# Optimization experiments

Measured on AMD Instinct MI355X. Metric: run time of the kernel, lower is better.

## Reference

```python
import jax, jax.numpy as jnp
import numpy as np

N = 6000          # num nodes (max_nodes)
E = 192000        # num edges
NTYPES = 100
NCLUST = 4        # hardcoded num_nodes=4 in diff_pool_net.__init__
OUT = 16
BN_EPS = 1e-5

PARAM_SHAPES = {
    'emb_w': (NTYPES, 64),
    # gnn1_pool: GNN(64, 64, 4, lin=True); DenseSAGEConv: lin_rel (no bias) + lin_root (bias)
    'pw1r': (64, 64), 'pw1l': (64, 64), 'pb1': (64,),
    'pw2r': (64, 64), 'pw2l': (64, 64), 'pb2': (64,),
    'pw3r': (NCLUST, 64), 'pw3l': (NCLUST, 64), 'pb3': (NCLUST,),
    'plin_w': (NCLUST, 2 * 64 + NCLUST), 'plin_b': (NCLUST,),
    # gnn1_embed: GNN(64, 64, 64, lin=False)
    'ew1r': (64, 64), 'ew1l': (64, 64), 'eb1': (64,),
    'ew2r': (64, 64), 'ew2l': (64, 64), 'eb2': (64,),
    'ew3r': (64, 64), 'ew3l': (64, 64), 'eb3': (64,),
    'lin1_w': (64, 192), 'lin1_b': (64,),
    'lin2_w': (OUT, 64), 'lin2_b': (OUT,),
    'embl_w': (32, 192), 'embl_b': (32,),
    'lin3_w': (OUT, 32 + OUT), 'lin3_b': (OUT,),
}


def _lin(x, w, b=None):
    y = x @ w.T
    return y if b is None else y + b


def _sage(x, adj, wr, wl, b):
    # DenseSAGEConv: mean-aggregate over dense adj, then lin_rel(agg) + lin_root(x)
    agg = jnp.matmul(adj, x)
    deg = jnp.clip(jnp.sum(adj, axis=-1, keepdims=True), 1.0, None)
    return _lin(agg / deg, wr) + _lin(x, wl, b)


def _bn(x):
    # training-mode BatchNorm1d with default gamma=1, beta=0 (biased variance)
    c = x.shape[-1]
    xf = x.reshape(-1, c)
    m = jnp.mean(xf, axis=0)
    v = jnp.var(xf, axis=0)
    return ((xf - m) * jax.lax.rsqrt(v + BN_EPS)).reshape(x.shape)


def _gnn(x, adj, wr1, wl1, b1, wr2, wl2, b2, wr3, wl3, b3, lw=None, lb=None):
    x1 = _bn(jax.nn.relu(_sage(x, adj, wr1, wl1, b1)))
    x2 = _bn(jax.nn.relu(_sage(x1, adj, wr2, wl2, b2)))
    x3 = _bn(jax.nn.relu(_sage(x2, adj, wr3, wl3, b3)))
    xc = jnp.concatenate([x1, x2, x3], axis=-1)
    if lw is not None:
        xc = jax.nn.relu(_lin(xc, lw, lb))
    return xc


def _forward(p, edge_index, node_types):
    # to_dense_adj: scatter-add edges into a dense [1, N, N] adjacency
    adj = jnp.zeros((N, N), jnp.float32).at[edge_index[0], edge_index[1]].add(1.0)[None]
    x = p['emb_w'][node_types][None]                      # [1, N, 64]
    s = _gnn(x, adj, p['pw1r'], p['pw1l'], p['pb1'],
             p['pw2r'], p['pw2l'], p['pb2'],
             p['pw3r'], p['pw3l'], p['pb3'],
             p['plin_w'], p['plin_b'])                    # [1, N, 4]
    xe = _gnn(x, adj, p['ew1r'], p['ew1l'], p['eb1'],
              p['ew2r'], p['ew2l'], p['eb2'],
              p['ew3r'], p['ew3l'], p['eb3'])             # [1, N, 192]
    x_embed = _lin(xe, p['embl_w'], p['embl_b'])          # [1, N, 32]
    # dense_diff_pool pooled features: softmax(S)^T @ X (pooled adj/losses are unused downstream)
    ssm = jax.nn.softmax(s, axis=-1)
    s_x = jnp.einsum('bnk,bnc->bkc', ssm, xe)             # [1, 4, 192]
    s_x = jax.nn.relu(_lin(s_x, p['lin1_w'], p['lin1_b']))
    s_x = _lin(s_x, p['lin2_w'], p['lin2_b'])             # [1, 4, OUT]
    # one_hot=True branch: per-node gather of its cluster row (vectorized form of the python loop)
    idx = jnp.argmax(s, axis=-1)                          # [1, N]
    res = jnp.take(s_x[0], idx[0], axis=0)[None]          # [1, N, OUT]
    return _lin(jnp.concatenate([x_embed, res], axis=-1), p['lin3_w'], p['lin3_b'])


def setup_inputs() -> dict:
    key = jax.random.key(0)
    ks = jax.random.split(key, len(PARAM_SHAPES) + 2)
    inp = {n: jax.random.normal(k, shp, jnp.float32) * 0.1
           for (n, shp), k in zip(PARAM_SHAPES.items(), ks)}
    inp['edge_index'] = jax.random.randint(ks[-2], (2, E), 0, N)
    inp['node_types'] = jax.random.randint(ks[-1], (N,), 0, NTYPES)
    return inp


def reference(edge_index, node_types, emb_w, pw1r, pw1l, pb1, pw2r, pw2l, pb2,
              pw3r, pw3l, pb3, plin_w, plin_b, ew1r, ew1l, eb1, ew2r, ew2l, eb2,
              ew3r, ew3l, eb3, lin1_w, lin1_b, lin2_w, lin2_b, embl_w, embl_b,
              lin3_w, lin3_b):
    args = locals()
    p = {k: args[k] for k in PARAM_SHAPES}
    return _forward(p, edge_index, node_types)
```

## Files before the change

### kernel.cpp

```cpp
#include <hip/hip_runtime.h>
#include <hip/hip_bf16.h>

#define NN 6000
#define EE 192000

#define W_DEG     0
#define W_CUR     6000
#define W_STATS   12000
#define W_SXACC   12768
#define W_ZEND    13536
#define W_FLAG    13536
#define W_ROWPTR  13540
#define W_COL     19544
#define W_X0      211544
#define W_ZP1     595544
#define W_ZP2     979544
#define W_ZP3     1363544
#define W_ZE1     1387544
#define W_ZE2     1771544
#define W_ZE3     2155544
#define W_S       2539544
#define W_SX2     2563544
#define W_PAR     2563608

struct PtrTab {
  const void* src[29];
  int off[29];
  int cnt[29];
};

__device__ __forceinline__ float bf2f(unsigned short h) {
  return __uint_as_float(((unsigned)h) << 16);
}
__device__ __forceinline__ int rfl(int x) { return __builtin_amdgcn_readfirstlane(x); }

__global__ void k_detect(const void* emb, int* flag) {
  __shared__ int bad;
  if (threadIdx.x == 0) bad = 0;
  __syncthreads();
  const unsigned short* p = (const unsigned short*)emb;
  float v0 = bf2f(p[threadIdx.x]);
  float v1 = bf2f(p[threadIdx.x + 256]);
  if (!(fabsf(v0) <= 100.f) || !(fabsf(v1) <= 100.f)) bad = 1;
  __syncthreads();
  if (threadIdx.x == 0) flag[0] = bad ? 0 : 1;
}

__global__ void k_convert(PtrTab tab, float* base, const int* flag) {
  int b = blockIdx.x;
  const void* s = tab.src[b];
  float* d = base + tab.off[b];
  int n = tab.cnt[b];
  bool bf = (flag[0] == 1);
  if (bf) {
    const unsigned short* sp = (const unsigned short*)s;
    for (int i = threadIdx.x; i < n; i += 256) d[i] = bf2f(sp[i]);
  } else {
    const float* sp = (const float*)s;
    for (int i = threadIdx.x; i < n; i += 256) d[i] = sp[i];
  }
}

__global__ void k_deg(const int* __restrict__ ei, int* __restrict__ deg) {
  int e = blockIdx.x * 256 + threadIdx.x;
  if (e < EE) atomicAdd(&deg[ei[e]], 1);
}

__global__ void k_scan(const int* __restrict__ deg, int* __restrict__ rowptr) {
  __shared__ int part[1024];
  int t = threadIdx.x;
  int base = t * 6;
  int loc[6]; int s = 0;
#pragma unroll
  for (int j = 0; j < 6; ++j) { int i = base + j; int v = (i < NN) ? deg[i] : 0; loc[j] = s; s += v; }
  part[t] = s;
  __syncthreads();
  for (int off = 1; off < 1024; off <<= 1) {
    int v = part[t];
    int add = (t >= off) ? part[t - off] : 0;
    __syncthreads();
    part[t] = v + add;
    __syncthreads();
  }
  int pre = (t == 0) ? 0 : part[t - 1];
#pragma unroll
  for (int j = 0; j < 6; ++j) { int i = base + j; if (i <= NN) rowptr[i] = pre + loc[j]; }
}

__global__ void k_scatter(const int* __restrict__ ei, const int* __restrict__ rowptr,
                          int* __restrict__ cur, int* __restrict__ col) {
  int e = blockIdx.x * 256 + threadIdx.x;
  if (e < EE) {
    int s = ei[e], d = ei[EE + e];
    int pos = atomicAdd(&cur[s], 1);
    col[rowptr[s] + pos] = d;
  }
}

__global__ void k_emb(const float* __restrict__ emb, const int* __restrict__ nt, float* __restrict__ x0) {
  int t = blockIdx.x * 256 + threadIdx.x;
  int i = t >> 4, q = t & 15;
  *(float4*)&x0[i * 64 + q * 4] = *(const float4*)&emb[nt[i] * 64 + q * 4];
}

template <int OUT, bool HS>
__device__ __forceinline__ void sage_body(
    const float* __restrict__ in_z, const float* __restrict__ in_stats,
    const float* __restrict__ wr, const float* __restrict__ wl, const float* __restrict__ bias,
    const int* __restrict__ rowptr, const int* __restrict__ col,
    float* __restrict__ out_z, float* __restrict__ out_stats,
    int vb, int total_waves,
    float* __restrict__ wrT, float* __restrict__ wlT, float* __restrict__ bs,
    float (* __restrict__ vec)[2][64], float (* __restrict__ red)[2][64]) {
  int tid = threadIdx.x, lane = tid & 63, wv = tid >> 6;

  for (int i = tid; i < 64 * OUT; i += 256) {
    int f = i >> 6, k = i & 63;
    wrT[k * (OUT + 1) + f] = wr[i];
    wlT[k * (OUT + 1) + f] = wl[i];
  }
  if (tid < OUT) bs[tid] = bias[tid];

  int quad = lane & 15, sub = lane >> 4;
  float m = 0.f, r = 1.f;
  float m4x = 0.f, m4y = 0.f, m4z = 0.f, m4w = 0.f;
  float r4x = 1.f, r4y = 1.f, r4z = 1.f, r4w = 1.f;
  if (HS) {
    float s = in_stats[lane], q = in_stats[64 + lane];
    m = s * (1.f / NN);
    r = rsqrtf(q * (1.f / NN) - m * m + 1e-5f);
    float4 s4 = *(const float4*)(in_stats + quad * 4);
    float4 q4 = *(const float4*)(in_stats + 64 + quad * 4);
    m4x = s4.x * (1.f / NN); m4y = s4.y * (1.f / NN); m4z = s4.z * (1.f / NN); m4w = s4.w * (1.f / NN);
    r4x = rsqrtf(q4.x * (1.f / NN) - m4x * m4x + 1e-5f);
    r4y = rsqrtf(q4.y * (1.f / NN) - m4y * m4y + 1e-5f);
    r4z = rsqrtf(q4.z * (1.f / NN) - m4z * m4z + 1e-5f);
    r4w = rsqrtf(q4.w * (1.f / NN) - m4w * m4w + 1e-5f);
  }
  __syncthreads();

  float accs = 0.f, accq = 0.f;
  int ol = lane & (OUT - 1);
  int wave_id = vb * 4 + wv;
  for (int n = wave_id; n < NN; n += total_waves) {
    float x = (in_z[n * 64 + lane] - m) * r;
    int rs = rfl(rowptr[n]), re = rfl(rowptr[n + 1]);
    int cnt = re - rs;
    float szx = 0.f, szy = 0.f, szz = 0.f, szw = 0.f;
    for (int base = rs; base < re; base += 32) {
#pragma unroll
      for (int u = 0; u < 8; ++u) {
        int cidx = base + u * 4 + sub;
        bool ok = cidx < re;
        int cc = ok ? cidx : rs;
        int j = col[cc];
        const float4 v = *(const float4*)(in_z + j * 64 + quad * 4);
        if (ok) { szx += v.x; szy += v.y; szz += v.z; szw += v.w; }
      }
    }
#pragma unroll
    for (int off = 16; off < 64; off <<= 1) {
      szx += __shfl_xor(szx, off);
      szy += __shfl_xor(szy, off);
      szz += __shfl_xor(szz, off);
      szw += __shfl_xor(szw, off);
    }
    float inv = 1.f / (float)(cnt > 0 ? cnt : 1);
    float fc = (float)cnt;
    if (sub == 0) {
      float4 a;
      a.x = (szx - fc * m4x) * r4x * inv;
      a.y = (szy - fc * m4y) * r4y * inv;
      a.z = (szz - fc * m4z) * r4z * inv;
      a.w = (szw - fc * m4w) * r4w * inv;
      *(float4*)&vec[wv][0][quad * 4] = a;
    }
    vec[wv][1][lane] = x;
    float y = bs[ol];
    const float* va = &vec[wv][0][0];
    const float* vx = &vec[wv][1][0];
#pragma unroll
    for (int kk = 0; kk < 16; ++kk) {
      const float4 a4 = *(const float4*)(va + kk * 4);
      const float4 x4 = *(const float4*)(vx + kk * 4);
      int k0 = kk * 4;
      y += a4.x * wrT[(k0 + 0) * (OUT + 1) + ol] + x4.x * wlT[(k0 + 0) * (OUT + 1) + ol];
      y += a4.y * wrT[(k0 + 1) * (OUT + 1) + ol] + x4.y * wlT[(k0 + 1) * (OUT + 1) + ol];
      y += a4.z * wrT[(k0 + 2) * (OUT + 1) + ol] + x4.z * wlT[(k0 + 2) * (OUT + 1) + ol];
      y += a4.w * wrT[(k0 + 3) * (OUT + 1) + ol] + x4.w * wlT[(k0 + 3) * (OUT + 1) + ol];
    }
    float z = fmaxf(y, 0.f);
    if (lane < OUT) {
      out_z[n * OUT + lane] = z;
      accs += z; accq += z * z;
    }
  }
  if (lane < OUT) { red[wv][0][lane] = accs; red[wv][1][lane] = accq; }
  __syncthreads();
  if (tid < OUT) {
    float s = red[0][0][tid] + red[1][0][tid] + red[2][0][tid] + red[3][0][tid];
    float q = red[0][1][tid] + red[1][1][tid] + red[2][1][tid] + red[3][1][tid];
    atomicAdd(&out_stats[tid], s);
    atomicAdd(&out_stats[64 + tid], q);
  }
}

template <int OUTA, int OUTB, bool HS>
__global__ __launch_bounds__(256, 4) void k_dual(
    const float* __restrict__ inA, const float* __restrict__ stA,
    const float* __restrict__ wrA, const float* __restrict__ wlA, const float* __restrict__ bA,
    float* __restrict__ outA, float* __restrict__ ostA,
    const float* __restrict__ inB, const float* __restrict__ stB,
    const float* __restrict__ wrB, const float* __restrict__ wlB, const float* __restrict__ bB,
    float* __restrict__ outB, float* __restrict__ ostB,
    const int* __restrict__ rowptr, const int* __restrict__ col, int G) {
  __shared__ float wrT[64 * 65];
  __shared__ float wlT[64 * 65];
  __shared__ float bs[64];
  __shared__ float vec[4][2][64];
  __shared__ float red[4][2][64];
  if ((int)blockIdx.x < G)
    sage_body<OUTA, HS>(inA, stA, wrA, wlA, bA, rowptr, col, outA, ostA,
                        blockIdx.x, G * 4, wrT, wlT, bs, vec, red);
  else
    sage_body<OUTB, HS>(inB, stB, wrB, wlB, bB, rowptr, col, outB, ostB,
                        blockIdx.x - G, G * 4, wrT, wlT, bs, vec, red);
}

__global__ __launch_bounds__(256) void k_pool(
    const float* __restrict__ zp1, const float* __restrict__ zp2, const float* __restrict__ zp3,
    const float* __restrict__ sp1, const float* __restrict__ sp2, const float* __restrict__ sp3,
    const float* __restrict__ ze1, const float* __restrict__ ze2, const float* __restrict__ ze3,
    const float* __restrict__ se1, const float* __restrict__ se2, const float* __restrict__ se3,
    const float* __restrict__ plw, const float* __restrict__ plb,
    float* __restrict__ s_out, float* __restrict__ sx_acc) {
  __shared__ float red[4][12][64];
  int tid = threadIdx.x, lane = tid & 63, wv = tid >> 6;

  float mp1 = sp1[lane] * (1.f / NN); float rp1 = rsqrtf(sp1[64 + lane] * (1.f / NN) - mp1 * mp1 + 1e-5f);
  float mp2 = sp2[lane] * (1.f / NN); float rp2 = rsqrtf(sp2[64 + lane] * (1.f / NN) - mp2 * mp2 + 1e-5f);
  float mp3 = 0.f, rp3 = 1.f;
  if (lane < 4) { mp3 = sp3[lane] * (1.f / NN); rp3 = rsqrtf(sp3[64 + lane] * (1.f / NN) - mp3 * mp3 + 1e-5f); }
  float me1 = se1[lane] * (1.f / NN); float re1 = rsqrtf(se1[64 + lane] * (1.f / NN) - me1 * me1 + 1e-5f);
  float me2 = se2[lane] * (1.f / NN); float re2 = rsqrtf(se2[64 + lane] * (1.f / NN) - me2 * me2 + 1e-5f);
  float me3 = se3[lane] * (1.f / NN); float re3 = rsqrtf(se3[64 + lane] * (1.f / NN) - me3 * me3 + 1e-5f);

  float w0a = plw[0 * 132 + lane], w0b = plw[0 * 132 + 64 + lane], w0c = (lane < 4) ? plw[0 * 132 + 128 + lane] : 0.f;
  float w1a = plw[1 * 132 + lane], w1b = plw[1 * 132 + 64 + lane], w1c = (lane < 4) ? plw[1 * 132 + 128 + lane] : 0.f;
  float w2a = plw[2 * 132 + lane], w2b = plw[2 * 132 + 64 + lane], w2c = (lane < 4) ? plw[2 * 132 + 128 + lane] : 0.f;
  float w3a = plw[3 * 132 + lane], w3b = plw[3 * 132 + 64 + lane], w3c = (lane < 4) ? plw[3 * 132 + 128 + lane] : 0.f;
  float pb0 = plb[0], pb1v = plb[1], pb2v = plb[2], pb3v = plb[3];

  float acc[12];
#pragma unroll
  for (int u = 0; u < 12; ++u) acc[u] = 0.f;

  int wave_id = blockIdx.x * 4 + wv;
  for (int n = wave_id; n < NN; n += 1500) {
    float a = (zp1[n * 64 + lane] - mp1) * rp1;
    float b = (zp2[n * 64 + lane] - mp2) * rp2;
    float c = (lane < 4) ? ((zp3[n * 4 + lane] - mp3) * rp3) : 0.f;
    float p0 = a * w0a + b * w0b + c * w0c;
    float p1 = a * w1a + b * w1b + c * w1c;
    float p2 = a * w2a + b * w2b + c * w2c;
    float p3 = a * w3a + b * w3b + c * w3c;
#pragma unroll
    for (int off = 1; off < 64; off <<= 1) {
      p0 += __shfl_xor(p0, off);
      p1 += __shfl_xor(p1, off);
      p2 += __shfl_xor(p2, off);
      p3 += __shfl_xor(p3, off);
    }
    float s0 = fmaxf(p0 + pb0, 0.f), s1 = fmaxf(p1 + pb1v, 0.f);
    float s2 = fmaxf(p2 + pb2v, 0.f), s3 = fmaxf(p3 + pb3v, 0.f);
    if (lane < 4) {
      float sv = (lane == 0) ? s0 : (lane == 1) ? s1 : (lane == 2) ? s2 : s3;
      s_out[n * 4 + lane] = sv;
    }
    float mx = fmaxf(fmaxf(s0, s1), fmaxf(s2, s3));
    float e0 = __expf(s0 - mx), e1 = __expf(s1 - mx), e2 = __expf(s2 - mx), e3 = __expf(s3 - mx);
    float inv = 1.f / (e0 + e1 + e2 + e3);
    e0 *= inv; e1 *= inv; e2 *= inv; e3 *= inv;
    float x1 = (ze1[n * 64 + lane] - me1) * re1;
    float x2 = (ze2[n * 64 + lane] - me2) * re2;
    float x3 = (ze3[n * 64 + lane] - me3) * re3;
    acc[0] += e0 * x1; acc[1] += e0 * x2; acc[2] += e0 * x3;
    acc[3] += e1 * x1; acc[4] += e1 * x2; acc[5] += e1 * x3;
    acc[6] += e2 * x1; acc[7] += e2 * x2; acc[8] += e2 * x3;
    acc[9] += e3 * x1; acc[10] += e3 * x2; acc[11] += e3 * x3;
  }
#pragma unroll
  for (int u = 0; u < 12; ++u) red[wv][u][lane] = acc[u];
  __syncthreads();
  for (int u = tid; u < 768; u += 256) {
    int f = u & 63, q = u >> 6;
    float v = red[0][q][f] + red[1][q][f] + red[2][q][f] + red[3][q][f];
    int k = q / 3, slot = q - 3 * k;
    atomicAdd(&sx_acc[k * 192 + slot * 64 + f], v);
  }
}

__global__ void k_mlp(const float* __restrict__ sx, const float* __restrict__ l1w, const float* __restrict__ l1b,
                      const float* __restrict__ l2w, const float* __restrict__ l2b, float* __restrict__ sx2) {
  __shared__ float tl[4][64];
  int tid = threadIdx.x;
  int k = tid >> 6, f = tid & 63;
  float v = l1b[f];
  for (int c = 0; c < 192; ++c) v += sx[k * 192 + c] * l1w[f * 192 + c];
  tl[k][f] = fmaxf(v, 0.f);
  __syncthreads();
  if (tid < 64) {
    int kk = tid >> 4, o = tid & 15;
    float u = l2b[o];
#pragma unroll
    for (int j = 0; j < 64; ++j) u += tl[kk][j] * l2w[o * 64 + j];
    sx2[kk * 16 + o] = u;
  }
}

__global__ __launch_bounds__(256) void k_final(
    const float* __restrict__ ze1, const float* __restrict__ ze2, const float* __restrict__ ze3,
    const float* __restrict__ se1, const float* __restrict__ se2, const float* __restrict__ se3,
    const float* __restrict__ ew, const float* __restrict__ ebv,
    const float* __restrict__ l3w, const float* __restrict__ l3b,
    const float* __restrict__ s_out, const float* __restrict__ sx2,
    const int* __restrict__ flag, void* __restrict__ out) {
  __shared__ float ewT[192 * 33];
  __shared__ float l3T[48 * 17];
  __shared__ float ebs[32], l3bs[16];
  __shared__ float xev[4][192];
  __shared__ float xed[4][32];
  int tid = threadIdx.x, lane = tid & 63, wv = tid >> 6;

  for (int i = tid; i < 6144; i += 256) { int cp = i / 192, c = i - cp * 192; ewT[c * 33 + cp] = ew[i]; }
  for (int i = tid; i < 768; i += 256) { int o = i / 48, j = i - o * 48; l3T[j * 17 + o] = l3w[i]; }
  if (tid < 32) ebs[tid] = ebv[tid];
  if (tid < 16) l3bs[tid] = l3b[tid];

  float me1 = se1[lane] * (1.f / NN); float re1 = rsqrtf(se1[64 + lane] * (1.f / NN) - me1 * me1 + 1e-5f);
  float me2 = se2[lane] * (1.f / NN); float re2 = rsqrtf(se2[64 + lane] * (1.f / NN) - me2 * me2 + 1e-5f);
  float me3 = se3[lane] * (1.f / NN); float re3 = rsqrtf(se3[64 + lane] * (1.f / NN) - me3 * me3 + 1e-5f);
  bool bf = (flag[0] == 1);
  __syncthreads();

  int h = lane >> 5, L = lane & 31;
  int wave_id = blockIdx.x * 4 + wv;
  for (int n = wave_id; n < NN; n += 2048) {
    float x1 = (ze1[n * 64 + lane] - me1) * re1;
    float x2 = (ze2[n * 64 + lane] - me2) * re2;
    float x3 = (ze3[n * 64 + lane] - me3) * re3;
    xev[wv][lane] = x1;
    xev[wv][64 + lane] = x2;
    xev[wv][128 + lane] = x3;
    float v = (h == 0) ? ebs[L] : 0.f;
    int cb = h * 96;
#pragma unroll
    for (int c4 = 0; c4 < 24; ++c4) {
      const float4 xv = *(const float4*)&xev[wv][cb + c4 * 4];
      int c0 = cb + c4 * 4;
      v += xv.x * ewT[(c0 + 0) * 33 + L];
      v += xv.y * ewT[(c0 + 1) * 33 + L];
      v += xv.z * ewT[(c0 + 2) * 33 + L];
      v += xv.w * ewT[(c0 + 3) * 33 + L];
    }
    v += __shfl_xor(v, 32);
    if (h == 0) xed[wv][L] = v;
    if (lane < 16) {
      int idx = 0; float best = s_out[n * 4 + 0];
      float c1 = s_out[n * 4 + 1]; if (c1 > best) { best = c1; idx = 1; }
      float c2 = s_out[n * 4 + 2]; if (c2 > best) { best = c2; idx = 2; }
      float c3 = s_out[n * 4 + 3]; if (c3 > best) { best = c3; idx = 3; }
      float racc = l3bs[lane];
#pragma unroll
      for (int j = 0; j < 32; ++j) racc += xed[wv][j] * l3T[j * 17 + lane];
      const float* sxr = sx2 + idx * 16;
#pragma unroll
      for (int j = 0; j < 16; ++j) racc += sxr[j] * l3T[(32 + j) * 17 + lane];
      if (bf) ((__hip_bfloat16*)out)[n * 16 + lane] = __float2bfloat16(racc);
      else    ((float*)out)[n * 16 + lane] = racc;
    }
  }
}

extern "C" void kernel_launch(void* const* d_in, const int* in_sizes, int n_in,
                              void* d_out, int out_size, void* d_ws, size_t ws_size,
                              hipStream_t stream) {
  float* F = (float*)d_ws;
  int* I = (int*)d_ws;

  static const int pcnt[29] = {6400, 4096, 4096, 64, 4096, 4096, 64, 256, 256, 4, 528, 4,
                               4096, 4096, 64, 4096, 4096, 64, 4096, 4096, 64,
                               12288, 64, 1024, 16, 6144, 32, 768, 16};
  int poff[29];
  { int a = 0; for (int i = 0; i < 29; ++i) { poff[i] = a; a += pcnt[i]; } }

  PtrTab tab;
  for (int i = 0; i < 29; ++i) { tab.src[i] = d_in[i]; tab.off[i] = poff[i]; tab.cnt[i] = pcnt[i]; }

  const int* ei = (const int*)d_in[29];
  const int* nt = (const int*)d_in[30];

  int* deg = I + W_DEG;
  int* cur = I + W_CUR;
  int* rowptr = I + W_ROWPTR;
  int* col = I + W_COL;
  int* flag = I + W_FLAG;
  float* st = F + W_STATS;
  float* sxacc = F + W_SXACC;
  float* x0 = F + W_X0;
  float* zp1 = F + W_ZP1; float* zp2 = F + W_ZP2; float* zp3 = F + W_ZP3;
  float* ze1 = F + W_ZE1; float* ze2 = F + W_ZE2; float* ze3 = F + W_ZE3;
  float* sbuf = F + W_S;
  float* sx2 = F + W_SX2;
  float* P = F + W_PAR;
#define PP(i) (P + poff[i])

  hipMemsetAsync(d_ws, 0, (size_t)W_ZEND * 4, stream);
  k_detect<<<1, 256, 0, stream>>>(d_in[0], flag);
  k_convert<<<29, 256, 0, stream>>>(tab, P, flag);
  k_deg<<<750, 256, 0, stream>>>(ei, deg);
  k_scan<<<1, 1024, 0, stream>>>(deg, rowptr);
  k_scatter<<<750, 256, 0, stream>>>(ei, rowptr, cur, col);
  k_emb<<<375, 256, 0, stream>>>(PP(0), nt, x0);

  k_dual<64, 64, false><<<1024, 256, 0, stream>>>(
      x0, nullptr, PP(1), PP(2), PP(3), zp1, st + 0 * 128,
      x0, nullptr, PP(12), PP(13), PP(14), ze1, st + 3 * 128,
      rowptr, col, 512);
  k_dual<64, 64, true><<<1024, 256, 0, stream>>>(
      zp1, st + 0 * 128, PP(4), PP(5), PP(6), zp2, st + 1 * 128,
      ze1, st + 3 * 128, PP(15), PP(16), PP(17), ze2, st + 4 * 128,
      rowptr, col, 512);
  k_dual<4, 64, true><<<1024, 256, 0, stream>>>(
      zp2, st + 1 * 128, PP(7), PP(8), PP(9), zp3, st + 2 * 128,
      ze2, st + 4 * 128, PP(18), PP(19), PP(20), ze3, st + 5 * 128,
      rowptr, col, 512);

  k_pool<<<375, 256, 0, stream>>>(zp1, zp2, zp3, st + 0 * 128, st + 1 * 128, st + 2 * 128,
                                  ze1, ze2, ze3, st + 3 * 128, st + 4 * 128, st + 5 * 128,
                                  PP(10), PP(11), sbuf, sxacc);
  k_mlp<<<1, 256, 0, stream>>>(sxacc, PP(21), PP(22), PP(23), PP(24), sx2);
  k_final<<<512, 256, 0, stream>>>(ze1, ze2, ze3, st + 3 * 128, st + 4 * 128, st + 5 * 128,
                                   PP(25), PP(26), PP(27), PP(28), sbuf, sx2, flag, d_out);
}
```

Baseline: 327.6 us.

## Pack SAGE weights for float4 LDS reads, interleave dual-branch blocks, nontemporal stores

```diff
diff --git a/kernel.cpp b/kernel.cpp
--- a/kernel.cpp
+++ b/kernel.cpp
@@ -110,14 +110,15 @@
     const int* __restrict__ rowptr, const int* __restrict__ col,
     float* __restrict__ out_z, float* __restrict__ out_stats,
     int vb, int total_waves,
-    float* __restrict__ wrT, float* __restrict__ wlT, float* __restrict__ bs,
+    float* __restrict__ wrP, float* __restrict__ wlP, float* __restrict__ bs,
     float (* __restrict__ vec)[2][64], float (* __restrict__ red)[2][64]) {
   int tid = threadIdx.x, lane = tid & 63, wv = tid >> 6;
 
   for (int i = tid; i < 64 * OUT; i += 256) {
     int f = i >> 6, k = i & 63;
-    wrT[k * (OUT + 1) + f] = wr[i];
-    wlT[k * (OUT + 1) + f] = wl[i];
+    int d = ((k >> 2) * OUT + f) * 4 + (k & 3);
+    wrP[d] = wr[i];
+    wlP[d] = wl[i];
   }
   if (tid < OUT) bs[tid] = bias[tid];
 
@@ -183,15 +184,16 @@
     for (int kk = 0; kk < 16; ++kk) {
       const float4 a4 = *(const float4*)(va + kk * 4);
       const float4 x4 = *(const float4*)(vx + kk * 4);
-      int k0 = kk * 4;
-      y += a4.x * wrT[(k0 + 0) * (OUT + 1) + ol] + x4.x * wlT[(k0 + 0) * (OUT + 1) + ol];
-      y += a4.y * wrT[(k0 + 1) * (OUT + 1) + ol] + x4.y * wlT[(k0 + 1) * (OUT + 1) + ol];
-      y += a4.z * wrT[(k0 + 2) * (OUT + 1) + ol] + x4.z * wlT[(k0 + 2) * (OUT + 1) + ol];
-      y += a4.w * wrT[(k0 + 3) * (OUT + 1) + ol] + x4.w * wlT[(k0 + 3) * (OUT + 1) + ol];
+      const float4 w4r = *(const float4*)&wrP[(kk * OUT + ol) * 4];
+      const float4 w4l = *(const float4*)&wlP[(kk * OUT + ol) * 4];
+      y += a4.x * w4r.x + x4.x * w4l.x;
+      y += a4.y * w4r.y + x4.y * w4l.y;
+      y += a4.z * w4r.z + x4.z * w4l.z;
+      y += a4.w * w4r.w + x4.w * w4l.w;
     }
     float z = fmaxf(y, 0.f);
     if (lane < OUT) {
-      out_z[n * OUT + lane] = z;
+      __builtin_nontemporal_store(z, &out_z[n * OUT + lane]);
       accs += z; accq += z * z;
     }
   }
@@ -214,17 +216,20 @@
     const float* __restrict__ wrB, const float* __restrict__ wlB, const float* __restrict__ bB,
     float* __restrict__ outB, float* __restrict__ ostB,
     const int* __restrict__ rowptr, const int* __restrict__ col, int G) {
-  __shared__ float wrT[64 * 65];
-  __shared__ float wlT[64 * 65];
+  __shared__ float wrP[64 * 64];
+  __shared__ float wlP[64 * 64];
   __shared__ float bs[64];
   __shared__ float vec[4][2][64];
   __shared__ float red[4][2][64];
-  if ((int)blockIdx.x < G)
+  int bx = (int)blockIdx.x;
+  int hi = (bx >> 2) & 1;
+  int vb = (bx >> 3) * 4 + (bx & 3);
+  if (hi == 0)
     sage_body<OUTA, HS>(inA, stA, wrA, wlA, bA, rowptr, col, outA, ostA,
-                        blockIdx.x, G * 4, wrT, wlT, bs, vec, red);
+                        vb, G * 4, wrP, wlP, bs, vec, red);
   else
     sage_body<OUTB, HS>(inB, stB, wrB, wlB, bB, rowptr, col, outB, ostB,
-                        blockIdx.x - G, G * 4, wrT, wlT, bs, vec, red);
+                        vb, G * 4, wrP, wlP, bs, vec, red);
 }
 
 __global__ __launch_bounds__(256) void k_pool(
```

New measurement: 341.7 us. 1.04x slower.

## Process two nodes per wave in SAGE gather and interleave dual-branch blocks

Applied to the files above, without the earlier changes.

```diff
diff --git a/kernel.cpp b/kernel.cpp
--- a/kernel.cpp
+++ b/kernel.cpp
@@ -111,7 +111,7 @@
     float* __restrict__ out_z, float* __restrict__ out_stats,
     int vb, int total_waves,
     float* __restrict__ wrT, float* __restrict__ wlT, float* __restrict__ bs,
-    float (* __restrict__ vec)[2][64], float (* __restrict__ red)[2][64]) {
+    float (* __restrict__ vec)[4][64], float (* __restrict__ red)[2][64]) {
   int tid = threadIdx.x, lane = tid & 63, wv = tid >> 6;
 
   for (int i = tid; i < 64 * OUT; i += 256) {
@@ -142,57 +142,93 @@
   float accs = 0.f, accq = 0.f;
   int ol = lane & (OUT - 1);
   int wave_id = vb * 4 + wv;
-  for (int n = wave_id; n < NN; n += total_waves) {
-    float x = (in_z[n * 64 + lane] - m) * r;
-    int rs = rfl(rowptr[n]), re = rfl(rowptr[n + 1]);
-    int cnt = re - rs;
-    float szx = 0.f, szy = 0.f, szz = 0.f, szw = 0.f;
-    for (int base = rs; base < re; base += 32) {
+  for (int n0 = wave_id; n0 < NN; n0 += 2 * total_waves) {
+    int n1 = n0 + total_waves;
+    bool has1 = n1 < NN;
+    float x0v = (in_z[n0 * 64 + lane] - m) * r;
+    float x1v = has1 ? (in_z[n1 * 64 + lane] - m) * r : 0.f;
+    int rs0 = rfl(rowptr[n0]), re0 = rfl(rowptr[n0 + 1]);
+    int rs1 = 0, re1 = 0;
+    if (has1) { rs1 = rfl(rowptr[n1]); re1 = rfl(rowptr[n1 + 1]); }
+    int cnt0 = re0 - rs0, cnt1 = re1 - rs1;
+    int it0 = (cnt0 + 31) >> 5, it1 = (cnt1 + 31) >> 5;
+    int iters = it0 > it1 ? it0 : it1;
+    float s0x = 0.f, s0y = 0.f, s0z = 0.f, s0w = 0.f;
+    float s1x = 0.f, s1y = 0.f, s1z = 0.f, s1w = 0.f;
+    for (int it = 0; it < iters; ++it) {
+      int b0 = rs0 + (it << 5), b1 = rs1 + (it << 5);
 #pragma unroll
       for (int u = 0; u < 8; ++u) {
-        int cidx = base + u * 4 + sub;
-        bool ok = cidx < re;
-        int cc = ok ? cidx : rs;
-        int j = col[cc];
-        const float4 v = *(const float4*)(in_z + j * 64 + quad * 4);
-        if (ok) { szx += v.x; szy += v.y; szz += v.z; szw += v.w; }
+        int ci0 = b0 + u * 4 + sub;
+        bool ok0 = ci0 < re0;
+        int j0 = col[ok0 ? ci0 : 0];
+        const float4 v0 = *(const float4*)(in_z + j0 * 64 + quad * 4);
+        int ci1 = b1 + u * 4 + sub;
+        bool ok1 = ci1 < re1;
+        int j1 = col[ok1 ? ci1 : 0];
+        const float4 v1 = *(const float4*)(in_z + j1 * 64 + quad * 4);
+        if (ok0) { s0x += v0.x; s0y += v0.y; s0z += v0.z; s0w += v0.w; }
+        if (ok1) { s1x += v1.x; s1y += v1.y; s1z += v1.z; s1w += v1.w; }
       }
     }
 #pragma unroll
     for (int off = 16; off < 64; off <<= 1) {
-      szx += __shfl_xor(szx, off);
-      szy += __shfl_xor(szy, off);
-      szz += __shfl_xor(szz, off);
-      szw += __shfl_xor(szw, off);
-    }
-    float inv = 1.f / (float)(cnt > 0 ? cnt : 1);
-    float fc = (float)cnt;
+      s0x += __shfl_xor(s0x, off);
+      s0y += __shfl_xor(s0y, off);
+      s0z += __shfl_xor(s0z, off);
+      s0w += __shfl_xor(s0w, off);
+      s1x += __shfl_xor(s1x, off);
+      s1y += __shfl_xor(s1y, off);
+      s1z += __shfl_xor(s1z, off);
+      s1w += __shfl_xor(s1w, off);
+    }
+    float inv0 = 1.f / (float)(cnt0 > 0 ? cnt0 : 1); float fc0 = (float)cnt0;
+    float inv1 = 1.f / (float)(cnt1 > 0 ? cnt1 : 1); float fc1 = (float)cnt1;
     if (sub == 0) {
       float4 a;
-      a.x = (szx - fc * m4x) * r4x * inv;
-      a.y = (szy - fc * m4y) * r4y * inv;
-      a.z = (szz - fc * m4z) * r4z * inv;
-      a.w = (szw - fc * m4w) * r4w * inv;
+      a.x = (s0x - fc0 * m4x) * r4x * inv0;
+      a.y = (s0y - fc0 * m4y) * r4y * inv0;
+      a.z = (s0z - fc0 * m4z) * r4z * inv0;
+      a.w = (s0w - fc0 * m4w) * r4w * inv0;
       *(float4*)&vec[wv][0][quad * 4] = a;
-    }
-    vec[wv][1][lane] = x;
-    float y = bs[ol];
-    const float* va = &vec[wv][0][0];
-    const float* vx = &vec[wv][1][0];
+      float4 b;
+      b.x = (s1x - fc1 * m4x) * r4x * inv1;
+      b.y = (s1y - fc1 * m4y) * r4y * inv1;
+      b.z = (s1z - fc1 * m4z) * r4z * inv1;
+      b.w = (s1w - fc1 * m4w) * r4w * inv1;
+      *(float4*)&vec[wv][2][quad * 4] = b;
+    }
+    vec[wv][1][lane] = x0v;
+    vec[wv][3][lane] = x1v;
+    float y0 = bs[ol], y1 = bs[ol];
+    const float* va0 = &vec[wv][0][0];
+    const float* vx0 = &vec[wv][1][0];
+    const float* va1 = &vec[wv][2][0];
+    const float* vx1 = &vec[wv][3][0];
 #pragma unroll
     for (int kk = 0; kk < 16; ++kk) {
-      const float4 a4 = *(const float4*)(va + kk * 4);
-      const float4 x4 = *(const float4*)(vx + kk * 4);
+      const float4 a0 = *(const float4*)(va0 + kk * 4);
+      const float4 q0 = *(const float4*)(vx0 + kk * 4);
+      const float4 a1 = *(const float4*)(va1 + kk * 4);
+      const float4 q1 = *(const float4*)(vx1 + kk * 4);
       int k0 = kk * 4;
-      y += a4.x * wrT[(k0 + 0) * (OUT + 1) + ol] + x4.x * wlT[(k0 + 0) * (OUT + 1) + ol];
-      y += a4.y * wrT[(k0 + 1) * (OUT + 1) + ol] + x4.y * wlT[(k0 + 1) * (OUT + 1) + ol];
-      y += a4.z * wrT[(k0 + 2) * (OUT + 1) + ol] + x4.z * wlT[(k0 + 2) * (OUT + 1) + ol];
-      y += a4.w * wrT[(k0 + 3) * (OUT + 1) + ol] + x4.w * wlT[(k0 + 3) * (OUT + 1) + ol];
-    }
-    float z = fmaxf(y, 0.f);
+      float wr0 = wrT[(k0 + 0) * (OUT + 1) + ol], wl0 = wlT[(k0 + 0) * (OUT + 1) + ol];
+      float wr1 = wrT[(k0 + 1) * (OUT + 1) + ol], wl1 = wlT[(k0 + 1) * (OUT + 1) + ol];
+      float wr2 = wrT[(k0 + 2) * (OUT + 1) + ol], wl2 = wlT[(k0 + 2) * (OUT + 1) + ol];
+      float wr3 = wrT[(k0 + 3) * (OUT + 1) + ol], wl3 = wlT[(k0 + 3) * (OUT + 1) + ol];
+      y0 += a0.x * wr0 + q0.x * wl0;  y1 += a1.x * wr0 + q1.x * wl0;
+      y0 += a0.y * wr1 + q0.y * wl1;  y1 += a1.y * wr1 + q1.y * wl1;
+      y0 += a0.z * wr2 + q0.z * wl2;  y1 += a1.z * wr2 + q1.z * wl2;
+      y0 += a0.w * wr3 + q0.w * wl3;  y1 += a1.w * wr3 + q1.w * wl3;
+    }
+    float z0 = fmaxf(y0, 0.f), z1 = fmaxf(y1, 0.f);
     if (lane < OUT) {
-      out_z[n * OUT + lane] = z;
-      accs += z; accq += z * z;
+      __builtin_nontemporal_store(z0, &out_z[n0 * OUT + lane]);
+      accs += z0; accq += z0 * z0;
+      if (has1) {
+        __builtin_nontemporal_store(z1, &out_z[n1 * OUT + lane]);
+        accs += z1; accq += z1 * z1;
+      }
     }
   }
   if (lane < OUT) { red[wv][0][lane] = accs; red[wv][1][lane] = accq; }
@@ -217,14 +253,17 @@
   __shared__ float wrT[64 * 65];
   __shared__ float wlT[64 * 65];
   __shared__ float bs[64];
-  __shared__ float vec[4][2][64];
+  __shared__ float vec[4][4][64];
   __shared__ float red[4][2][64];
-  if ((int)blockIdx.x < G)
+  int bx = (int)blockIdx.x;
+  int hi = (bx >> 2) & 1;
+  int vb = (bx >> 3) * 4 + (bx & 3);
+  if (hi == 0)
     sage_body<OUTA, HS>(inA, stA, wrA, wlA, bA, rowptr, col, outA, ostA,
-                        blockIdx.x, G * 4, wrT, wlT, bs, vec, red);
+                        vb, G * 4, wrT, wlT, bs, vec, red);
   else
     sage_body<OUTB, HS>(inB, stB, wrB, wlB, bB, rowptr, col, outB, ostB,
-                        blockIdx.x - G, G * 4, wrT, wlT, bs, vec, red);
+                        vb, G * 4, wrT, wlT, bs, vec, red);
 }
 
 __global__ __launch_bounds__(256) void k_pool(
```

New measurement: 368.6 us. 12.5% more time.

## Gather neighbors with wave-wide readlane broadcast and interleave dual-branch block mapping

Applied to the files above, without the earlier changes.

```diff
diff --git a/kernel.cpp b/kernel.cpp
--- a/kernel.cpp
+++ b/kernel.cpp
@@ -121,21 +121,11 @@
   }
   if (tid < OUT) bs[tid] = bias[tid];
 
-  int quad = lane & 15, sub = lane >> 4;
   float m = 0.f, r = 1.f;
-  float m4x = 0.f, m4y = 0.f, m4z = 0.f, m4w = 0.f;
-  float r4x = 1.f, r4y = 1.f, r4z = 1.f, r4w = 1.f;
   if (HS) {
     float s = in_stats[lane], q = in_stats[64 + lane];
     m = s * (1.f / NN);
     r = rsqrtf(q * (1.f / NN) - m * m + 1e-5f);
-    float4 s4 = *(const float4*)(in_stats + quad * 4);
-    float4 q4 = *(const float4*)(in_stats + 64 + quad * 4);
-    m4x = s4.x * (1.f / NN); m4y = s4.y * (1.f / NN); m4z = s4.z * (1.f / NN); m4w = s4.w * (1.f / NN);
-    r4x = rsqrtf(q4.x * (1.f / NN) - m4x * m4x + 1e-5f);
-    r4y = rsqrtf(q4.y * (1.f / NN) - m4y * m4y + 1e-5f);
-    r4z = rsqrtf(q4.z * (1.f / NN) - m4z * m4z + 1e-5f);
-    r4w = rsqrtf(q4.w * (1.f / NN) - m4w * m4w + 1e-5f);
   }
   __syncthreads();
 
@@ -146,35 +136,26 @@
     float x = (in_z[n * 64 + lane] - m) * r;
     int rs = rfl(rowptr[n]), re = rfl(rowptr[n + 1]);
     int cnt = re - rs;
-    float szx = 0.f, szy = 0.f, szz = 0.f, szw = 0.f;
-    for (int base = rs; base < re; base += 32) {
-#pragma unroll
-      for (int u = 0; u < 8; ++u) {
-        int cidx = base + u * 4 + sub;
-        bool ok = cidx < re;
-        int cc = ok ? cidx : rs;
-        int j = col[cc];
-        const float4 v = *(const float4*)(in_z + j * 64 + quad * 4);
-        if (ok) { szx += v.x; szy += v.y; szz += v.z; szw += v.w; }
+    float sz = 0.f;
+    for (int base = rs; base < re; base += 64) {
+      int ci = base + lane;
+      int colv = col[ci < re ? ci : (re - 1)];
+      int full = re - base; if (full > 64) full = 64;
+      int ng8 = (full + 7) >> 3;
+      for (int g = 0; g < ng8; ++g) {
+        int e0 = g * 8;
+#pragma unroll
+        for (int u = 0; u < 8; ++u) {
+          int j = __builtin_amdgcn_readlane(colv, e0 + u);
+          float v = in_z[j * 64 + lane];
+          sz += (e0 + u < full) ? v : 0.f;
+        }
       }
     }
-#pragma unroll
-    for (int off = 16; off < 64; off <<= 1) {
-      szx += __shfl_xor(szx, off);
-      szy += __shfl_xor(szy, off);
-      szz += __shfl_xor(szz, off);
-      szw += __shfl_xor(szw, off);
-    }
+    float fc = (float)cnt;
     float inv = 1.f / (float)(cnt > 0 ? cnt : 1);
-    float fc = (float)cnt;
-    if (sub == 0) {
-      float4 a;
-      a.x = (szx - fc * m4x) * r4x * inv;
-      a.y = (szy - fc * m4y) * r4y * inv;
-      a.z = (szz - fc * m4z) * r4z * inv;
-      a.w = (szw - fc * m4w) * r4w * inv;
-      *(float4*)&vec[wv][0][quad * 4] = a;
-    }
+    float a = (sz - fc * m) * r * inv;
+    vec[wv][0][lane] = a;
     vec[wv][1][lane] = x;
     float y = bs[ol];
     const float* va = &vec[wv][0][0];
@@ -219,12 +200,15 @@
   __shared__ float bs[64];
   __shared__ float vec[4][2][64];
   __shared__ float red[4][2][64];
-  if ((int)blockIdx.x < G)
+  int bx = (int)blockIdx.x;
+  int hi = (bx >> 2) & 1;
+  int vb = (bx >> 3) * 4 + (bx & 3);
+  if (hi == 0)
     sage_body<OUTA, HS>(inA, stA, wrA, wlA, bA, rowptr, col, outA, ostA,
-                        blockIdx.x, G * 4, wrT, wlT, bs, vec, red);
+                        vb, G * 4, wrT, wlT, bs, vec, red);
   else
     sage_body<OUTB, HS>(inB, stB, wrB, wlB, bB, rowptr, col, outB, ostB,
-                        blockIdx.x - G, G * 4, wrT, wlT, bs, vec, red);
+                        vb, G * 4, wrT, wlT, bs, vec, red);
 }
 
 __global__ __launch_bounds__(256) void k_pool(
```

Measured after the change: 291.6 us. 11.0% less time.
